# Kernel tuning notes

Measured on AMD Instinct MI355X. Metric: run time of the kernel, lower is better.

The kernel has to match this reference:

```python
import jax, jax.numpy as jnp
import numpy as np

H, W, K = 256, 256, 3          # three 256x256 operand label matrices (last is target)
N = K * H * W                  # total labels / logits per sample
LANE = 8                       # memory_lane_width
NROWS = N // LANE              # memory grid rows (N divisible by 8)
NOPS = H * W                   # one STORE op per target cell


def _staged(h, exp):
    # staged cache-penalty: base = h**exp scaled by cache-level factor
    base = jnp.power(h, exp)
    f = jnp.where(h <= 2.0, 1.0,
        jnp.where(h <= 4.0, 1.5,
        jnp.where(h <= 8.0, 2.0,
        jnp.where(h <= 16.0, 3.0, 5.0))))
    return jnp.sum(base * f, axis=-1)


def setup_inputs() -> dict:
    key = jax.random.key(0)
    ks = jax.random.split(key, 7)
    B = 8
    return {
        "mem_logits_batch": jax.random.normal(ks[0], (B, N), jnp.float32),
        "conv1_w": jax.random.normal(ks[1], (K * 8, 1, 3, 3), jnp.float32) * 0.02,
        "conv1_b": jax.random.normal(ks[2], (K * 8,), jnp.float32) * 0.02,
        "conv2_w": jax.random.normal(ks[3], (16, 8, 3, 3), jnp.float32) * 0.02,
        "conv2_b": jax.random.normal(ks[4], (16,), jnp.float32) * 0.02,
        "proj_w": jax.random.normal(ks[5], (NOPS, 16 * 4 * 4), jnp.float32) * 0.02,
        "proj_b": jax.random.normal(ks[6], (NOPS,), jnp.float32) * 0.02,
    }


def reference(mem_logits_batch, conv1_w, conv1_b, conv2_w, conv2_b, proj_w, proj_b):
    B = mem_logits_batch.shape[0]
    dn = ("NCHW", "OIHW", "NCHW")

    # addr_map: label i (labels are all distinct, contiguous per matrix) -> argsort(logits)[i]
    addr = jnp.argsort(mem_logits_batch, axis=-1)              # [B, N] permutation of 0..N-1

    # per-matrix address images; grouped conv = K independent 1->8 convs
    x = addr.astype(jnp.float32).reshape(B, K, H, W)           # [B, K, H, W]
    feat = jax.lax.conv_general_dilated(x, conv1_w, (1, 1), "SAME",
                                        dimension_numbers=dn, feature_group_count=K)
    feat = jax.nn.relu(feat + conv1_b[None, :, None, None])    # [B, K*8, H, W]

    # scatter feat columns into memory grid at their addresses.
    # addr is a full permutation -> scatter == gather with inverse permutation.
    feats_flat = feat.reshape(B, K, 8, H * W).transpose(0, 2, 1, 3).reshape(B, 8, N)
    inv = jnp.argsort(addr, axis=-1)                           # [B, N]
    mem = jnp.take_along_axis(feats_flat, inv[:, None, :], axis=2)
    mem = mem.reshape(B, 8, NROWS, LANE)                       # [B, 8, NROWS, 8]

    mem2 = jax.lax.conv_general_dilated(mem, conv2_w, (1, 1), "SAME", dimension_numbers=dn)
    mem2 = jax.nn.relu(mem2 + conv2_b[None, :, None, None])    # [B, 16, NROWS, 8]

    # AdaptiveAvgPool2d((4,4)): dims divisible -> uniform block mean
    pooled = mem2.reshape(B, 16, 4, NROWS // 4, 4, LANE // 4).mean(axis=(3, 5))  # [B,16,4,4]
    flat = pooled.reshape(B, 16 * 4 * 4)
    op_logits = flat @ proj_w.T + proj_b                       # [B, NOPS]

    # order operations by op logits; op t reads addr[k*HW+t] for sources, dst = last matrix
    perm = jnp.argsort(op_logits, axis=-1)                     # [B, NOPS]
    S = addr.reshape(B, K, NOPS).transpose(0, 2, 1)            # [B, NOPS, K] = [src0, src1, dst]
    S_ord = jnp.take_along_axis(S, perm[:, :, None], axis=1).astype(jnp.float32)

    # intra-op hops: along each op's [src..., dst] sequence
    intra_d = (S_ord[:, :, 1:] - S_ord[:, :, :-1]).reshape(B, -1)   # [B, NOPS*(K-1)]
    # inter-op hops: first addr of op minus dst addr of previous op
    inter_d = S_ord[:, 1:, 0] - S_ord[:, :-1, -1]                   # [B, NOPS-1]

    intra_pen = _staged(jax.nn.relu(intra_d), 1.0) + _staged(jax.nn.relu(-intra_d), 2.0)
    inter_pen = _staged(jax.nn.relu(inter_d), 1.0) + _staged(jax.nn.relu(-inter_d), 2.0)
    return inter_pen, intra_pen
```

## Files before the change

### kernel.cpp

```cpp
#include <hip/hip_runtime.h>
#include <stdint.h>

typedef unsigned int u32;
typedef unsigned long long u64;

#define BN 8
#define HW_ 65536
#define N1 196608
#define NOPS_ 65536
#define NROWS_ 24576
#define NB1 192
#define NB2 64

__device__ __forceinline__ u32 fkey(float x) {
  u32 u = __float_as_uint(x);
  return u ^ ((u & 0x80000000u) ? 0xFFFFFFFFu : 0x80000000u);
}

template <bool FIRST>
__global__ __launch_bounds__(256) void rs_hist(const u64* __restrict__ kv, const float* __restrict__ xf,
                                               u32* __restrict__ hist, u32* __restrict__ gTot,
                                               int n, int nblk, int shift) {
  __shared__ u32 h[256];
  int t = threadIdx.x;
  int b = blockIdx.x / nblk, blk = blockIdx.x % nblk;
  h[t] = 0;
  __syncthreads();
  if (FIRST) {
    const float* xp = xf + (size_t)b * n + (size_t)blk * 1024;
#pragma unroll
    for (int j = 0; j < 4; ++j) {
      u32 d = fkey(xp[j * 256 + t]) & 255u;
      atomicAdd(&h[d], 1u);
    }
  } else {
    const u64* kp = kv + (size_t)b * n + (size_t)blk * 1024;
#pragma unroll
    for (int j = 0; j < 4; ++j) {
      u32 d = (u32)(kp[j * 256 + t] >> (32 + shift)) & 255u;
      atomicAdd(&h[d], 1u);
    }
  }
  __syncthreads();
  hist[((size_t)b * 256 + t) * nblk + blk] = h[t];
  atomicAdd(&gTot[b * 256 + t], h[t]);
}

__device__ __forceinline__ u32 wscan_incl(u32 x, int lane) {
#pragma unroll
  for (int off = 1; off < 64; off <<= 1) {
    u32 y = __shfl_up(x, off, 64);
    if (lane >= off) x += y;
  }
  return x;
}

__global__ __launch_bounds__(256) void rs_scanB(u32* __restrict__ hist, const u32* __restrict__ gTot, int nblk) {
  int t = threadIdx.x, w = t >> 6, lane = t & 63;
  int b = blockIdx.x >> 6, dgrp = blockIdx.x & 63;
  int d = dgrp * 4 + w;
  const u32* gt = gTot + b * 256;
  u32 base = 0, run = 0;
  int dc = d >> 6, dl = d & 63;
#pragma unroll
  for (int c = 0; c < 4; ++c) {
    u32 v = gt[c * 64 + lane];
    u32 incl = wscan_incl(v, lane);
    if (c == dc) base = run + __shfl(incl - v, dl, 64);
    run += __shfl(incl, 63, 64);
  }
  u32* p = hist + ((size_t)b * 256 + d) * nblk;
  u32 acc = base;
  for (int c = 0; c < nblk; c += 64) {
    u32 v = p[c + lane];
    u32 incl = wscan_incl(v, lane);
    p[c + lane] = acc + incl - v;
    acc += __shfl(incl, 63, 64);
  }
}

template <bool FIRST, bool FINAL>
__global__ __launch_bounds__(256) void rs_scatter(const u64* __restrict__ kvIn, const float* __restrict__ xf,
                                                  u64* __restrict__ out64, u32* __restrict__ out32,
                                                  const u32* __restrict__ hist, int n, int nblk, int shift) {
  __shared__ u32 sBase[256];
  __shared__ u32 cnt[16][256];
  int t = threadIdx.x, lane = t & 63, wid = t >> 6;
  int b = blockIdx.x / nblk, blk = blockIdx.x % nblk;
  u64 kvr[4]; u32 dg[4];
  if (FIRST) {
    const float* xp = xf + (size_t)b * n + (size_t)blk * 1024;
#pragma unroll
    for (int j = 0; j < 4; ++j) {
      u32 k = fkey(xp[j * 256 + t]);
      kvr[j] = ((u64)k << 32) | (u32)(blk * 1024 + j * 256 + t);
      dg[j] = k & 255u;
    }
  } else {
    const u64* kp = kvIn + (size_t)b * n + (size_t)blk * 1024;
#pragma unroll
    for (int j = 0; j < 4; ++j) {
      kvr[j] = kp[j * 256 + t];
      dg[j] = (u32)(kvr[j] >> (32 + shift)) & 255u;
    }
  }
  sBase[t] = hist[((size_t)b * 256 + t) * nblk + blk];
#pragma unroll
  for (int r = 0; r < 16; ++r) cnt[r][t] = 0;
  __syncthreads();
  u64 lmask = (1ull << lane) - 1ull;
  u32 rw[4];
#pragma unroll
  for (int j = 0; j < 4; ++j) {
    u32 d = dg[j];
    u64 peers = ~0ull;
#pragma unroll
    for (int bit = 0; bit < 8; ++bit) {
      u64 bal = __ballot((d >> bit) & 1);
      peers &= ((d >> bit) & 1) ? bal : ~bal;
    }
    u64 lower = peers & lmask;
    rw[j] = (u32)__popcll(lower);
    if (lower == 0) cnt[j * 4 + wid][d] = (u32)__popcll(peers);
  }
  __syncthreads();
  u32 run = sBase[t];
#pragma unroll
  for (int r = 0; r < 16; ++r) { u32 c = cnt[r][t]; cnt[r][t] = run; run += c; }
  __syncthreads();
#pragma unroll
  for (int j = 0; j < 4; ++j) {
    u32 pos = cnt[j * 4 + wid][dg[j]] + rw[j];
    if (FINAL) out32[(size_t)b * n + pos] = (u32)kvr[j];
    else out64[(size_t)b * n + pos] = kvr[j];
  }
}

__global__ __launch_bounds__(256) void conv1_scatter(const u32* __restrict__ addr, const float* __restrict__ w1,
                                                     const float* __restrict__ b1, float* __restrict__ mem,
                                                     uint4* __restrict__ addr3) {
  __shared__ float ax[34][34];
  __shared__ float ws[8][9];
  __shared__ float bs[8];
  int t = threadIdx.x;
  int blk = blockIdx.x;
  int tile = blk & 63; int bk2 = blk >> 6; int k = bk2 % 3; int b = bk2 / 3;
  int ty = tile >> 3, tx = tile & 7;
  if (t < 72) ws[t / 9][t % 9] = w1[k * 72 + t];
  if (t >= 128 && t < 136) bs[t - 128] = b1[k * 8 + (t - 128)];
  const u32* ap = addr + (size_t)b * N1 + (size_t)k * HW_;
  for (int idx = t; idx < 34 * 34; idx += 256) {
    int y = idx / 34, x = idx % 34;
    int h = ty * 32 + y - 1, w = tx * 32 + x - 1;
    float v = 0.f;
    if (h >= 0 && h < 256 && w >= 0 && w < 256) v = (float)ap[h * 256 + w];
    ax[y][x] = v;
  }
  __syncthreads();
  float* mb = mem + (size_t)b * N1 * 8;
  const u32* adb = addr + (size_t)b * N1;
  uint4* a3b = addr3 + (size_t)b * HW_;
#pragma unroll
  for (int s = 0; s < 4; ++s) {
    int p = t + s * 256;
    int y = p >> 5, x = p & 31;
    float f[8];
#pragma unroll
    for (int c = 0; c < 8; ++c) f[c] = bs[c];
#pragma unroll
    for (int dy = 0; dy < 3; ++dy)
#pragma unroll
      for (int dx = 0; dx < 3; ++dx) {
        float v = ax[y + dy][x + dx];
#pragma unroll
        for (int c = 0; c < 8; ++c) f[c] = fmaf(ws[c][dy * 3 + dx], v, f[c]);
      }
    u32 a = (u32)ax[y + 1][x + 1];
    float4* dst = reinterpret_cast<float4*>(mb + (size_t)a * 8);
    float4 lo = make_float4(fmaxf(f[0], 0.f), fmaxf(f[1], 0.f), fmaxf(f[2], 0.f), fmaxf(f[3], 0.f));
    float4 hi = make_float4(fmaxf(f[4], 0.f), fmaxf(f[5], 0.f), fmaxf(f[6], 0.f), fmaxf(f[7], 0.f));
    dst[0] = lo; dst[1] = hi;
    if (k == 0) {
      int gp = (ty * 32 + y) * 256 + tx * 32 + x;
      a3b[gp] = make_uint4(a, adb[HW_ + gp], adb[2 * HW_ + gp], 0u);
    }
  }
}

__global__ __launch_bounds__(256, 3) void c2p1(const float* __restrict__ mem, const float* __restrict__ w2,
                                               const float* __restrict__ b2, float* __restrict__ gPartial) {
  __shared__ float tile[98 * 68];
  __shared__ float w2s[1152];
  __shared__ float b2s[16];
  __shared__ float red[16][64];
  int blk = blockIdx.x; int sub = blk & 255; int b = blk >> 8;
  int r0 = sub * 96;
  int t = threadIdx.x;
  for (int idx = t; idx < 1152; idx += 256) w2s[idx] = w2[idx];
  if (t < 16) b2s[t] = b2[t];
  const float* mb = mem + (size_t)b * (N1 * 8);
  for (int q = t; q < 98 * 16; q += 256) {
    int ti = q >> 4, qw = q & 15;
    int r = r0 - 1 + ti;
    float4 v = make_float4(0.f, 0.f, 0.f, 0.f);
    if (r >= 0 && r < NROWS_) v = *reinterpret_cast<const float4*>(mb + (size_t)r * 64 + qw * 4);
    *reinterpret_cast<float4*>(&tile[ti * 68 + qw * 4]) = v;
  }
  __syncthreads();
  int co = t & 15, rowgrp = t >> 4;
  float wreg[3][3][8];
#pragma unroll
  for (int ci = 0; ci < 8; ++ci)
#pragma unroll
    for (int kr = 0; kr < 3; ++kr)
#pragma unroll
      for (int kc = 0; kc < 3; ++kc)
        wreg[kr][kc][ci] = w2s[(co * 8 + ci) * 9 + kr * 3 + kc];
  float bias = b2s[co];
  float pool[4] = {0.f, 0.f, 0.f, 0.f};
#define CSTEP(V, CI) do { \
    if (j < 3) { \
      if (li >= 1) s0[li - 1] = fmaf((V), wreg[j][2][CI], s0[li - 1]); \
      s0[li] = fmaf((V), wreg[j][1][CI], s0[li]); \
      if (li < 7) s0[li + 1] = fmaf((V), wreg[j][0][CI], s0[li + 1]); \
    } \
    if (j >= 1) { \
      if (li >= 1) s1[li - 1] = fmaf((V), wreg[j - 1][2][CI], s1[li - 1]); \
      s1[li] = fmaf((V), wreg[j - 1][1][CI], s1[li]); \
      if (li < 7) s1[li + 1] = fmaf((V), wreg[j - 1][0][CI], s1[li + 1]); \
    } \
  } while (0)
#pragma unroll 1
  for (int i = 0; i < 3; ++i) {
    int lr0 = rowgrp * 2 + 32 * i;
    float s0[8], s1[8];
#pragma unroll
    for (int l = 0; l < 8; ++l) { s0[l] = 0.f; s1[l] = 0.f; }
#pragma unroll
    for (int j = 0; j < 4; ++j) {
      const float* trow = &tile[(lr0 + j) * 68];
#pragma unroll
      for (int li = 0; li < 8; ++li) {
        float4 aa = *reinterpret_cast<const float4*>(trow + li * 8);
        float4 bb = *reinterpret_cast<const float4*>(trow + li * 8 + 4);
        CSTEP(aa.x, 0); CSTEP(aa.y, 1); CSTEP(aa.z, 2); CSTEP(aa.w, 3);
        CSTEP(bb.x, 4); CSTEP(bb.y, 5); CSTEP(bb.z, 6); CSTEP(bb.w, 7);
      }
    }
#pragma unroll
    for (int l = 0; l < 8; ++l)
      pool[l >> 1] += fmaxf(s0[l] + bias, 0.f) + fmaxf(s1[l] + bias, 0.f);
  }
#undef CSTEP
#pragma unroll
  for (int lb = 0; lb < 4; ++lb) red[rowgrp][lb * 16 + co] = pool[lb];
  __syncthreads();
  if (t < 64) {
    float s = 0.f;
#pragma unroll
    for (int rg = 0; rg < 16; ++rg) s += red[rg][t];
    int rb = sub >> 6, subW = sub & 63;
    gPartial[(((size_t)(b * 4 + rb) * 64 + subW) * 64) + t] = s;
  }
}

__global__ void c2p2(const float* __restrict__ gPartial, float* __restrict__ flatS) {
  int b = blockIdx.x; int t = threadIdx.x;
  int ch = t >> 4; int rb = (t >> 2) & 3; int lb = t & 3;
  float s = 0.f;
  for (int sub = 0; sub < 64; ++sub)
    s += gPartial[(((size_t)(b * 4 + rb) * 64 + sub) * 64) + lb * 16 + ch];
  flatS[b * 256 + t] = s * (1.0f / 12288.0f);
}

__global__ __launch_bounds__(256) void proj_k(const float* __restrict__ flatS, const float* __restrict__ pw,
                                              const float* __restrict__ pb, u64* __restrict__ kv2) {
  __shared__ float fs[8][256];
  int t = threadIdx.x;
  for (int i = t; i < 2048; i += 256) fs[i >> 8][i & 255] = flatS[i];
  __syncthreads();
  int q = t & 15; int og = t >> 4;
  int o = blockIdx.x * 16 + og;
  float acc[8];
#pragma unroll
  for (int b = 0; b < 8; ++b) acc[b] = 0.f;
  const float* wr = pw + (size_t)o * 256;
#pragma unroll
  for (int j = 0; j < 16; ++j) {
    float w = wr[q + 16 * j];
#pragma unroll
    for (int b = 0; b < 8; ++b) acc[b] = fmaf(fs[b][q + 16 * j], w, acc[b]);
  }
#pragma unroll
  for (int m = 1; m < 16; m <<= 1)
#pragma unroll
    for (int b = 0; b < 8; ++b) acc[b] += __shfl_xor(acc[b], m, 64);
  if (q == 0) {
    float bias = pb[o];
#pragma unroll
    for (int b = 0; b < 8; ++b) {
      u32 k = fkey(acc[b] + bias);
      kv2[(size_t)b * NOPS_ + o] = ((u64)k << 32) | (u32)o;
    }
  }
}

__device__ __forceinline__ double stagedp(float d) {
  double h, base;
  if (d >= 0.f) { h = (double)d; base = h; }
  else { h = (double)(-d); base = h * h; }
  double f = (h <= 2.0) ? 1.0 : (h <= 4.0) ? 1.5 : (h <= 8.0) ? 2.0 : (h <= 16.0) ? 3.0 : 5.0;
  return base * f;
}

__global__ __launch_bounds__(256) void penalty_k(const u32* __restrict__ perm, const uint4* __restrict__ addr3,
                                                 double* __restrict__ partials, u32* __restrict__ ctr,
                                                 float* __restrict__ out) {
  int b = blockIdx.x >> 6; int blk = blockIdx.x & 63;
  int t = threadIdx.x, lane = t & 63;
  const u32* pm = perm + (size_t)b * NOPS_;
  const uint4* a3 = addr3 + (size_t)b * HW_;
  double intra = 0.0, inter = 0.0;
#pragma unroll
  for (int s = 0; s < 4; ++s) {
    int tg = blk * 1024 + s * 256 + t;
    u32 p = pm[tg];
    uint4 g = a3[p];
    float a0 = (float)g.x, a1 = (float)g.y, a2 = (float)g.z;
    intra += stagedp(a1 - a0) + stagedp(a2 - a1);
    float a2p = __shfl_up(a2, 1, 64);
    if (lane == 0 && tg > 0) {
      u32 pp = pm[tg - 1];
      a2p = (float)a3[pp].z;
    }
    if (tg > 0) inter += stagedp(a0 - a2p);
  }
#pragma unroll
  for (int m = 1; m < 64; m <<= 1) {
    intra += __shfl_xor(intra, m, 64);
    inter += __shfl_xor(inter, m, 64);
  }
  __shared__ double red[4][2];
  __shared__ u32 lastFlag;
  int wid = t >> 6;
  if (lane == 0) { red[wid][0] = inter; red[wid][1] = intra; }
  __syncthreads();
  if (t == 0) {
    double i0 = red[0][0] + red[1][0] + red[2][0] + red[3][0];
    double i1 = red[0][1] + red[1][1] + red[2][1] + red[3][1];
    partials[((size_t)b * 64 + blk) * 2 + 0] = i0;
    partials[((size_t)b * 64 + blk) * 2 + 1] = i1;
    __threadfence();
    u32 done = atomicAdd(ctr, 1u);
    lastFlag = (done == (u32)(BN * 64 - 1));
  }
  __syncthreads();
  if (lastFlag) {
    __threadfence();
    if (t < 16) {
      int which = t >> 3, bb = t & 7;
      double s = 0.0;
      for (int k = 0; k < 64; ++k) s += partials[((size_t)bb * 64 + k) * 2 + which];
      out[which * 8 + bb] = (float)s;
    }
  }
}

extern "C" void kernel_launch(void* const* d_in, const int* in_sizes, int n_in,
                              void* d_out, int out_size, void* d_ws, size_t ws_size,
                              hipStream_t stream) {
  const float* logits = (const float*)d_in[0];
  const float* w1 = (const float*)d_in[1];
  const float* b1 = (const float*)d_in[2];
  const float* w2 = (const float*)d_in[3];
  const float* b2 = (const float*)d_in[4];
  const float* pw = (const float*)d_in[5];
  const float* pb = (const float*)d_in[6];
  float* out = (float*)d_out;

  char* ws = (char*)d_ws;
  size_t o = 0;
  auto take = [&](size_t bytes) { char* p = ws + o; o += (bytes + 255) & ~(size_t)255; return p; };
  u64* kv1A = (u64*)take((size_t)BN * N1 * 8);
  u64* kv1B = (u64*)take((size_t)BN * N1 * 8);
  u64* kv2A = (u64*)take((size_t)BN * NOPS_ * 8);
  u64* kv2B = (u64*)take((size_t)BN * NOPS_ * 8);
  u32* hist = (u32*)take((size_t)256 * NB1 * BN * 4);
  u32* gTotAll = (u32*)take(((size_t)8 * BN * 256 + 64) * 4);
  u32* addr = (u32*)take((size_t)BN * N1 * 4);
  float* mem = (float*)take((size_t)BN * N1 * 8 * 4);
  float* gPartial = (float*)take((size_t)BN * 4 * 64 * 64 * 4);
  float* flatS = (float*)take((size_t)BN * 256 * 4);
  u32* perm = (u32*)take((size_t)BN * NOPS_ * 4);
  double* partials = (double*)take((size_t)BN * 64 * 2 * 8);
  uint4* addr3 = (uint4*)kv1A;
  u32* ctr = gTotAll + (size_t)8 * BN * 256;

  hipMemsetAsync(gTotAll, 0, ((size_t)8 * BN * 256 + 64) * 4, stream);

  {
    u32* gT = gTotAll;
    rs_hist<true><<<BN * NB1, 256, 0, stream>>>(nullptr, logits, hist, gT, N1, NB1, 0);
    rs_scanB<<<BN * 64, 256, 0, stream>>>(hist, gT, NB1);
    rs_scatter<true, false><<<BN * NB1, 256, 0, stream>>>(nullptr, logits, kv1B, nullptr, hist, N1, NB1, 0);
  }
  u64* src = kv1B; u64* dst = kv1A;
  for (int p = 1; p < 4; ++p) {
    u32* gT = gTotAll + (size_t)p * BN * 256;
    rs_hist<false><<<BN * NB1, 256, 0, stream>>>(src, nullptr, hist, gT, N1, NB1, p * 8);
    rs_scanB<<<BN * 64, 256, 0, stream>>>(hist, gT, NB1);
    if (p < 3) {
      rs_scatter<false, false><<<BN * NB1, 256, 0, stream>>>(src, nullptr, dst, nullptr, hist, N1, NB1, p * 8);
      u64* tmp = src; src = dst; dst = tmp;
    } else {
      rs_scatter<false, true><<<BN * NB1, 256, 0, stream>>>(src, nullptr, nullptr, addr, hist, N1, NB1, p * 8);
    }
  }

  conv1_scatter<<<BN * 3 * 64, 256, 0, stream>>>(addr, w1, b1, mem, addr3);

  c2p1<<<BN * 256, 256, 0, stream>>>(mem, w2, b2, gPartial);
  c2p2<<<BN, 256, 0, stream>>>(gPartial, flatS);

  proj_k<<<NOPS_ / 16, 256, 0, stream>>>(flatS, pw, pb, kv2A);

  src = kv2A; dst = kv2B;
  for (int p = 0; p < 4; ++p) {
    u32* gT = gTotAll + (size_t)(4 + p) * BN * 256;
    rs_hist<false><<<BN * NB2, 256, 0, stream>>>(src, nullptr, hist, gT, NOPS_, NB2, p * 8);
    rs_scanB<<<BN * 64, 256, 0, stream>>>(hist, gT, NB2);
    if (p < 3) {
      rs_scatter<false, false><<<BN * NB2, 256, 0, stream>>>(src, nullptr, dst, nullptr, hist, NOPS_, NB2, p * 8);
      u64* tmp = src; src = dst; dst = tmp;
    } else {
      rs_scatter<false, true><<<BN * NB2, 256, 0, stream>>>(src, nullptr, nullptr, perm, hist, NOPS_, NB2, p * 8);
    }
  }

  penalty_k<<<BN * 64, 256, 0, stream>>>(perm, addr3, partials, ctr, out);
}
```

Measured before the change: 294.5 us.

## Fuse next-pass radix histograms into scatter and projection kernels

Each radix scatter pass now builds the histogram for the next digit while writing its output, using global atomics keyed by the destination block, and proj_k builds the first-pass histogram for the op-logit sort. This removes six separate histogram kernels and their re-reads of the key arrays. Histogram and total buffers are carved from the not-yet-used mem buffer and zeroed by memsets. In exchange, the scatter adds global atomics with scattered addresses and extra shared-memory atomics, which may contend.

```diff
diff --git a/kernel.cpp b/kernel.cpp
--- a/kernel.cpp
+++ b/kernel.cpp
@@ -17,29 +17,18 @@
   return u ^ ((u & 0x80000000u) ? 0xFFFFFFFFu : 0x80000000u);
 }
 
-template <bool FIRST>
-__global__ __launch_bounds__(256) void rs_hist(const u64* __restrict__ kv, const float* __restrict__ xf,
-                                               u32* __restrict__ hist, u32* __restrict__ gTot,
-                                               int n, int nblk, int shift) {
+__global__ __launch_bounds__(256) void rs_hist0(const float* __restrict__ xf, u32* __restrict__ hist,
+                                                u32* __restrict__ gTot, int n, int nblk) {
   __shared__ u32 h[256];
   int t = threadIdx.x;
   int b = blockIdx.x / nblk, blk = blockIdx.x % nblk;
   h[t] = 0;
   __syncthreads();
-  if (FIRST) {
-    const float* xp = xf + (size_t)b * n + (size_t)blk * 1024;
-#pragma unroll
-    for (int j = 0; j < 4; ++j) {
-      u32 d = fkey(xp[j * 256 + t]) & 255u;
-      atomicAdd(&h[d], 1u);
-    }
-  } else {
-    const u64* kp = kv + (size_t)b * n + (size_t)blk * 1024;
-#pragma unroll
-    for (int j = 0; j < 4; ++j) {
-      u32 d = (u32)(kp[j * 256 + t] >> (32 + shift)) & 255u;
-      atomicAdd(&h[d], 1u);
-    }
+  const float* xp = xf + (size_t)b * n + (size_t)blk * 1024;
+#pragma unroll
+  for (int j = 0; j < 4; ++j) {
+    u32 d = fkey(xp[j * 256 + t]) & 255u;
+    atomicAdd(&h[d], 1u);
   }
   __syncthreads();
   hist[((size_t)b * 256 + t) * nblk + blk] = h[t];
@@ -79,12 +68,14 @@
   }
 }
 
-template <bool FIRST, bool FINAL>
+template <bool FIRST, bool FINAL, bool NEXT>
 __global__ __launch_bounds__(256) void rs_scatter(const u64* __restrict__ kvIn, const float* __restrict__ xf,
                                                   u64* __restrict__ out64, u32* __restrict__ out32,
-                                                  const u32* __restrict__ hist, int n, int nblk, int shift) {
+                                                  const u32* __restrict__ hist, u32* __restrict__ histN,
+                                                  u32* __restrict__ gTotN, int n, int nblk, int shift) {
   __shared__ u32 sBase[256];
   __shared__ u32 cnt[16][256];
+  __shared__ u32 hN[256];
   int t = threadIdx.x, lane = t & 63, wid = t >> 6;
   int b = blockIdx.x / nblk, blk = blockIdx.x % nblk;
   u64 kvr[4]; u32 dg[4];
@@ -105,6 +96,7 @@
     }
   }
   sBase[t] = hist[((size_t)b * 256 + t) * nblk + blk];
+  if (NEXT) hN[t] = 0;
 #pragma unroll
   for (int r = 0; r < 16; ++r) cnt[r][t] = 0;
   __syncthreads();
@@ -133,6 +125,16 @@
     u32 pos = cnt[j * 4 + wid][dg[j]] + rw[j];
     if (FINAL) out32[(size_t)b * n + pos] = (u32)kvr[j];
     else out64[(size_t)b * n + pos] = kvr[j];
+    if (NEXT) {
+      u32 dn = (u32)(kvr[j] >> (32 + shift + 8)) & 255u;
+      atomicAdd(&histN[((size_t)b * 256 + dn) * nblk + (pos >> 10)], 1u);
+      atomicAdd(&hN[dn], 1u);
+    }
+  }
+  if (NEXT) {
+    __syncthreads();
+    u32 v = hN[t];
+    if (v) atomicAdd(&gTotN[b * 256 + t], v);
   }
 }
 
@@ -274,7 +276,8 @@
 }
 
 __global__ __launch_bounds__(256) void proj_k(const float* __restrict__ flatS, const float* __restrict__ pw,
-                                              const float* __restrict__ pb, u64* __restrict__ kv2) {
+                                              const float* __restrict__ pb, u64* __restrict__ kv2,
+                                              u32* __restrict__ hist20, u32* __restrict__ gTot20) {
   __shared__ float fs[8][256];
   int t = threadIdx.x;
   for (int i = t; i < 2048; i += 256) fs[i >> 8][i & 255] = flatS[i];
@@ -297,10 +300,14 @@
     for (int b = 0; b < 8; ++b) acc[b] += __shfl_xor(acc[b], m, 64);
   if (q == 0) {
     float bias = pb[o];
+    int ob = blockIdx.x >> 6;
 #pragma unroll
     for (int b = 0; b < 8; ++b) {
       u32 k = fkey(acc[b] + bias);
       kv2[(size_t)b * NOPS_ + o] = ((u64)k << 32) | (u32)o;
+      u32 d0 = k & 255u;
+      atomicAdd(&hist20[((size_t)b * 256 + d0) * NB2 + ob], 1u);
+      atomicAdd(&gTot20[b * 256 + d0], 1u);
     }
   }
 }
@@ -385,8 +392,6 @@
   u64* kv1B = (u64*)take((size_t)BN * N1 * 8);
   u64* kv2A = (u64*)take((size_t)BN * NOPS_ * 8);
   u64* kv2B = (u64*)take((size_t)BN * NOPS_ * 8);
-  u32* hist = (u32*)take((size_t)256 * NB1 * BN * 4);
-  u32* gTotAll = (u32*)take(((size_t)8 * BN * 256 + 64) * 4);
   u32* addr = (u32*)take((size_t)BN * N1 * 4);
   float* mem = (float*)take((size_t)BN * N1 * 8 * 4);
   float* gPartial = (float*)take((size_t)BN * 4 * 64 * 64 * 4);
@@ -394,48 +399,49 @@
   u32* perm = (u32*)take((size_t)BN * NOPS_ * 4);
   double* partials = (double*)take((size_t)BN * 64 * 2 * 8);
   uint4* addr3 = (uint4*)kv1A;
-  u32* ctr = gTotAll + (size_t)8 * BN * 256;
-
-  hipMemsetAsync(gTotAll, 0, ((size_t)8 * BN * 256 + 64) * 4, stream);
-
-  {
-    u32* gT = gTotAll;
-    rs_hist<true><<<BN * NB1, 256, 0, stream>>>(nullptr, logits, hist, gT, N1, NB1, 0);
-    rs_scanB<<<BN * 64, 256, 0, stream>>>(hist, gT, NB1);
-    rs_scatter<true, false><<<BN * NB1, 256, 0, stream>>>(nullptr, logits, kv1B, nullptr, hist, N1, NB1, 0);
-  }
-  u64* src = kv1B; u64* dst = kv1A;
-  for (int p = 1; p < 4; ++p) {
-    u32* gT = gTotAll + (size_t)p * BN * 256;
-    rs_hist<false><<<BN * NB1, 256, 0, stream>>>(src, nullptr, hist, gT, N1, NB1, p * 8);
-    rs_scanB<<<BN * 64, 256, 0, stream>>>(hist, gT, NB1);
-    if (p < 3) {
-      rs_scatter<false, false><<<BN * NB1, 256, 0, stream>>>(src, nullptr, dst, nullptr, hist, N1, NB1, p * 8);
-      u64* tmp = src; src = dst; dst = tmp;
-    } else {
-      rs_scatter<false, true><<<BN * NB1, 256, 0, stream>>>(src, nullptr, nullptr, addr, hist, N1, NB1, p * 8);
-    }
-  }
+
+  const size_t HS1 = (size_t)256 * NB1 * BN;
+  const size_t HS2 = (size_t)256 * NB2 * BN;
+  const size_t GT = (size_t)BN * 256;
+  u32* memU = (u32*)mem;
+  u32* h1_[4]; u32* g1_[4]; u32* h2_[4]; u32* g2_[4];
+  for (int p = 0; p < 4; ++p) h1_[p] = memU + p * HS1;
+  for (int p = 0; p < 4; ++p) g1_[p] = memU + 4 * HS1 + p * GT;
+  u32* mid = memU + 4 * HS1 + 4 * GT;
+  for (int p = 0; p < 4; ++p) h2_[p] = mid + p * HS2;
+  for (int p = 0; p < 4; ++p) g2_[p] = mid + 4 * HS2 + p * GT;
+  u32* ctr = mid + 4 * HS2 + 4 * GT;
+
+  hipMemsetAsync(memU, 0, (4 * HS1 + 4 * GT) * 4, stream);
+
+  rs_hist0<<<BN * NB1, 256, 0, stream>>>(logits, h1_[0], g1_[0], N1, NB1);
+  rs_scanB<<<BN * 64, 256, 0, stream>>>(h1_[0], g1_[0], NB1);
+  rs_scatter<true, false, true><<<BN * NB1, 256, 0, stream>>>(nullptr, logits, kv1B, nullptr, h1_[0], h1_[1], g1_[1], N1, NB1, 0);
+  rs_scanB<<<BN * 64, 256, 0, stream>>>(h1_[1], g1_[1], NB1);
+  rs_scatter<false, false, true><<<BN * NB1, 256, 0, stream>>>(kv1B, nullptr, kv1A, nullptr, h1_[1], h1_[2], g1_[2], N1, NB1, 8);
+  rs_scanB<<<BN * 64, 256, 0, stream>>>(h1_[2], g1_[2], NB1);
+  rs_scatter<false, false, true><<<BN * NB1, 256, 0, stream>>>(kv1A, nullptr, kv1B, nullptr, h1_[2], h1_[3], g1_[3], N1, NB1, 16);
+  rs_scanB<<<BN * 64, 256, 0, stream>>>(h1_[3], g1_[3], NB1);
+  rs_scatter<false, true, false><<<BN * NB1, 256, 0, stream>>>(kv1B, nullptr, nullptr, addr, h1_[3], nullptr, nullptr, N1, NB1, 24);
 
   conv1_scatter<<<BN * 3 * 64, 256, 0, stream>>>(addr, w1, b1, mem, addr3);
 
   c2p1<<<BN * 256, 256, 0, stream>>>(mem, w2, b2, gPartial);
+
+  hipMemsetAsync(mid, 0, (4 * HS2 + 4 * GT + 64) * 4, stream);
+
   c2p2<<<BN, 256, 0, stream>>>(gPartial, flatS);
 
-  proj_k<<<NOPS_ / 16, 256, 0, stream>>>(flatS, pw, pb, kv2A);
-
-  src = kv2A; dst = kv2B;
-  for (int p = 0; p < 4; ++p) {
-    u32* gT = gTotAll + (size_t)(4 + p) * BN * 256;
-    rs_hist<false><<<BN * NB2, 256, 0, stream>>>(src, nullptr, hist, gT, NOPS_, NB2, p * 8);
-    rs_scanB<<<BN * 64, 256, 0, stream>>>(hist, gT, NB2);
-    if (p < 3) {
-      rs_scatter<false, false><<<BN * NB2, 256, 0, stream>>>(src, nullptr, dst, nullptr, hist, NOPS_, NB2, p * 8);
-      u64* tmp = src; src = dst; dst = tmp;
-    } else {
-      rs_scatter<false, true><<<BN * NB2, 256, 0, stream>>>(src, nullptr, nullptr, perm, hist, NOPS_, NB2, p * 8);
-    }
-  }
+  proj_k<<<NOPS_ / 16, 256, 0, stream>>>(flatS, pw, pb, kv2A, h2_[0], g2_[0]);
+
+  rs_scanB<<<BN * 64, 256, 0, stream>>>(h2_[0], g2_[0], NB2);
+  rs_scatter<false, false, true><<<BN * NB2, 256, 0, stream>>>(kv2A, nullptr, kv2B, nullptr, h2_[0], h2_[1], g2_[1], NOPS_, NB2, 0);
+  rs_scanB<<<BN * 64, 256, 0, stream>>>(h2_[1], g2_[1], NB2);
+  rs_scatter<false, false, true><<<BN * NB2, 256, 0, stream>>>(kv2B, nullptr, kv2A, nullptr, h2_[1], h2_[2], g2_[2], NOPS_, NB2, 8);
+  rs_scanB<<<BN * 64, 256, 0, stream>>>(h2_[2], g2_[2], NB2);
+  rs_scatter<false, false, true><<<BN * NB2, 256, 0, stream>>>(kv2A, nullptr, kv2B, nullptr, h2_[2], h2_[3], g2_[3], NOPS_, NB2, 16);
+  rs_scanB<<<BN * 64, 256, 0, stream>>>(h2_[3], g2_[3], NB2);
+  rs_scatter<false, true, false><<<BN * NB2, 256, 0, stream>>>(kv2B, nullptr, nullptr, perm, h2_[3], nullptr, nullptr, NOPS_, NB2, 24);
 
   penalty_k<<<BN * 64, 256, 0, stream>>>(perm, addr3, partials, ctr, out);
 }
```

Result: slower. 722.6 us (+145.4%).
